# Kernel optimization log

Hardware: AMD Instinct MI355X
Metric: run time of the kernel (lower is better)

Reference implementation:

```python
import jax, jax.numpy as jnp
import numpy as np

N_NODES = 100000
N_EDGES = 1600000  # undirected edges (incidence rows)
F_IN, HID, N_CLS = 500, 256, 40
K_ITERS = 5
LAMBDA1 = 3.0
LAMBDA2 = 3.0


def setup_inputs() -> dict:
    key = jax.random.key(0)
    k1, k2, k3, k4, k5 = jax.random.split(key, 5)
    x = jax.random.normal(k1, (N_NODES, F_IN), dtype=jnp.float32)
    W1 = jax.random.normal(k2, (F_IN, HID), dtype=jnp.float32) * 0.05
    W2 = jax.random.normal(k3, (HID, N_CLS), dtype=jnp.float32) * 0.05
    src = jax.random.randint(k4, (N_EDGES,), 0, N_NODES, dtype=jnp.int32)
    off = jax.random.randint(k5, (N_EDGES,), 1, N_NODES, dtype=jnp.int32)
    dst = (src + off) % N_NODES  # avoid self-edges
    return {"x": x, "W1": W1, "W2": W2, "src": src, "dst": dst}


def reference(x, W1, W2, src, dst):
    N = x.shape[0]
    # --- MLP (eval mode: dropout is identity) ---
    h = jnp.maximum(x @ W1, 0.0)
    h = h @ W2  # [N, C]

    # --- gcn_norm: A_hat = D^{-1/2}(A + I)D^{-1/2}, deg from A + I ---
    rows = jnp.concatenate([src, dst])  # symmetric adjacency
    cols = jnp.concatenate([dst, src])
    deg = jax.ops.segment_sum(jnp.ones(rows.shape[0], x.dtype), rows,
                              num_segments=N) + 1.0
    dis = deg ** -0.5  # deg_inv_sqrt, [N]
    edge_val = dis[rows] * dis[cols]
    self_val = dis * dis

    def spmm(v):  # A_hat @ v
        return (jax.ops.segment_sum(edge_val[:, None] * v[cols], rows,
                                    num_segments=N) + self_val[:, None] * v)

    # normalized incidence: inc[e, src]=dis[src], inc[e, dst]=-dis[dst]
    def inc_t(z):  # inc.T @ z -> [N, C]
        return dis[:, None] * (jax.ops.segment_sum(z, src, num_segments=N)
                               - jax.ops.segment_sum(z, dst, num_segments=N))

    def inc(v):  # inc @ v -> [E, C]
        vs = dis[:, None] * v
        return vs[src] - vs[dst]

    gamma = 1.0 / (1.0 + LAMBDA2)
    beta = 1.0 / (2.0 * gamma)

    hh = h
    xc = h
    z = jnp.zeros((src.shape[0], h.shape[1]), h.dtype)
    for _ in range(K_ITERS):
        y = gamma * hh + (1.0 - gamma) * spmm(xc)
        x_bar = y - gamma * inc_t(z)
        z_bar = z + beta * inc(x_bar)
        # L21 proximal projection: clamp row norms at lambda1
        rn = jnp.linalg.norm(z_bar, axis=1)
        scale = jnp.where(rn > 0,
                          jnp.minimum(rn, LAMBDA1) / jnp.where(rn > 0, rn, 1.0),
                          0.0)
        z = scale[:, None] * z_bar
        xc = y - gamma * inc_t(z)
        # F.dropout with training=False is identity
    return jax.nn.log_softmax(xc, axis=1)
```

## Files before the change

kernel.cpp:

```cpp
#include <hip/hip_runtime.h>
#include <hip/hip_fp16.h>
#include <math.h>

#define NN 100000
#define NE 1600000
#define FIN 500
#define FINP 512
#define HID 256
#define NC 40
#define NC2 20
#define KIT 5
#define L1P 3.0f
#define GAM 0.25f
#define BET 2.0f
#define OMG 0.75f
#define PADH2 32

typedef short bf16x8 __attribute__((ext_vector_type(8)));
typedef unsigned short us8 __attribute__((ext_vector_type(8)));
typedef float f32x4 __attribute__((ext_vector_type(4)));

__device__ inline void split_bf16(float x, unsigned short& hi, unsigned short& lo) {
    unsigned u = __float_as_uint(x);
    hi = (unsigned short)(u >> 16);
    float r = x - __uint_as_float(u & 0xFFFF0000u);
    unsigned ur = __float_as_uint(r);
    ur += 0x8000u + ((ur >> 16) & 1u);
    lo = (unsigned short)(ur >> 16);
}

__global__ void k_hist(const int* __restrict__ s, const int* __restrict__ d, int* cs, int* cd) {
    int e = blockIdx.x * 256 + threadIdx.x;
    if (e < NE) { atomicAdd(&cs[s[e]], 1); atomicAdd(&cd[d[e]], 1); }
}

__global__ void k_scan1(const int* __restrict__ cnt, int* rp, int* bs) {
    __shared__ int sm[1024];
    int i = blockIdx.x * 1024 + threadIdx.x;
    int v = (i < NN) ? cnt[i] : 0;
    sm[threadIdx.x] = v;
    __syncthreads();
    for (int off = 1; off < 1024; off <<= 1) {
        int t = (threadIdx.x >= off) ? sm[threadIdx.x - off] : 0;
        __syncthreads();
        sm[threadIdx.x] += t;
        __syncthreads();
    }
    if (i < NN) rp[i] = sm[threadIdx.x] - v;
    if (threadIdx.x == 1023) bs[blockIdx.x] = sm[1023];
}

__global__ void k_scan2(int* bs, int nb) {
    if (threadIdx.x == 0 && blockIdx.x == 0) {
        int run = 0;
        for (int j = 0; j < nb; j++) { int t = bs[j]; bs[j] = run; run += t; }
    }
}

__global__ void k_scan3(int* rp, const int* __restrict__ bs, int total) {
    int i = blockIdx.x * 1024 + threadIdx.x;
    if (i < NN) rp[i] += bs[blockIdx.x];
    if (i == 0) rp[NN] = total;
}

__global__ void k_dis(const int* __restrict__ cs, const int* __restrict__ cd, float* __restrict__ dis) {
    int n = blockIdx.x * 256 + threadIdx.x;
    if (n < NN) dis[n] = rsqrtf((float)(cs[n] + cd[n]) + 1.0f);
}

__global__ void k_fillp(const int* __restrict__ s, const int* __restrict__ d,
                        const int* __restrict__ rps, const int* __restrict__ rpd,
                        int* curs, int* curd,
                        int* sa, int* sb, int* pd, int* da) {
    int e = blockIdx.x * 256 + threadIdx.x;
    if (e < NE) {
        int a = s[e], b = d[e];
        int i = rps[a] + atomicAdd(&curs[a], 1);
        int j = rpd[b] + atomicAdd(&curd[b], 1);
        sa[i] = a; sb[i] = b; pd[i] = j; da[j] = a;
    }
}

__global__ void k_splitW(const float* __restrict__ W1, unsigned short* __restrict__ Wh,
                         unsigned short* __restrict__ Wl) {
    int idx = blockIdx.x * 256 + threadIdx.x;
    if (idx >= HID * FINP) return;
    int kk = idx >> 8;
    int n  = idx & (HID - 1);
    float v = (kk < FIN) ? W1[(size_t)kk * HID + n] : 0.f;
    unsigned short h, l;
    split_bf16(v, h, l);
    Wh[(size_t)n * FINP + kk] = h;
    Wl[(size_t)n * FINP + kk] = l;
}

__global__ __launch_bounds__(256) void k_gemm1m(const float* __restrict__ X,
                                                const unsigned short* __restrict__ W1h,
                                                const unsigned short* __restrict__ W1l,
                                                float* __restrict__ H1) {
    __shared__ unsigned short Ah[32][40], Al[32][40];
    __shared__ unsigned short Bh[256][40], Bl[256][40];
    const int t = threadIdx.x;
    const int rblk = blockIdx.x * 32;
    const int lane = t & 63, wv = t >> 6;
    const int mw = (wv >> 1) * 16;
    const int nw = (wv & 1) * 128;
    const int l15 = lane & 15, kg = lane >> 4;

    f32x4 acc[8];
    #pragma unroll
    for (int i = 0; i < 8; i++) acc[i] = (f32x4){0.f, 0.f, 0.f, 0.f};

    const int ar = t >> 3;
    const int ak = (t & 7) * 4;
    const int grow = rblk + ar;

    for (int ks = 0; ks < 16; ks++) {
        const int k0 = ks * 32;
        __syncthreads();
        {
            float4 v = make_float4(0.f, 0.f, 0.f, 0.f);
            if (grow < NN && k0 + ak < FIN)
                v = *(const float4*)(X + (size_t)grow * FIN + k0 + ak);
            ushort4 h4, l4;
            split_bf16(v.x, h4.x, l4.x); split_bf16(v.y, h4.y, l4.y);
            split_bf16(v.z, h4.z, l4.z); split_bf16(v.w, h4.w, l4.w);
            *(ushort4*)&Ah[ar][ak] = h4;
            *(ushort4*)&Al[ar][ak] = l4;
        }
        {
            const size_t wb = (size_t)t * FINP + k0;
            #pragma unroll
            for (int q = 0; q < 4; q++) {
                *(us8*)&Bh[t][q * 8] = *(const us8*)&W1h[wb + q * 8];
                *(us8*)&Bl[t][q * 8] = *(const us8*)&W1l[wb + q * 8];
            }
        }
        __syncthreads();
        bf16x8 a_h = *(const bf16x8*)&Ah[mw + l15][kg * 8];
        bf16x8 a_l = *(const bf16x8*)&Al[mw + l15][kg * 8];
        #pragma unroll
        for (int nt = 0; nt < 8; nt++) {
            int n = nw + nt * 16 + l15;
            bf16x8 b_h = *(const bf16x8*)&Bh[n][kg * 8];
            bf16x8 b_l = *(const bf16x8*)&Bl[n][kg * 8];
            acc[nt] = __builtin_amdgcn_mfma_f32_16x16x32_bf16(a_h, b_h, acc[nt], 0, 0, 0);
            acc[nt] = __builtin_amdgcn_mfma_f32_16x16x32_bf16(a_h, b_l, acc[nt], 0, 0, 0);
            acc[nt] = __builtin_amdgcn_mfma_f32_16x16x32_bf16(a_l, b_h, acc[nt], 0, 0, 0);
        }
    }
    const int orow = rblk + mw + kg * 4;
    #pragma unroll
    for (int reg = 0; reg < 4; reg++) {
        int gr = orow + reg;
        if (gr < NN) {
            #pragma unroll
            for (int nt = 0; nt < 8; nt++)
                H1[(size_t)gr * HID + nw + nt * 16 + l15] = fmaxf(acc[nt][reg], 0.f);
        }
    }
}

__global__ __launch_bounds__(256) void k_gemm2(const float* __restrict__ H1,
                                               const float* __restrict__ W2,
                                               const float* __restrict__ dis,
                                               float* __restrict__ hh, __half2* __restrict__ xg2) {
    __shared__ float w2s[HID * NC];
    for (int i = threadIdx.x; i < HID * NC; i += 256) w2s[i] = W2[i];
    __syncthreads();
    int wave = threadIdx.x >> 6, lane = threadIdx.x & 63;
    int n = blockIdx.x * 4 + wave;
    if (n >= NN) return;
    if (lane < NC) {
        const float* hr = H1 + (size_t)n * HID;
        float acc = 0.f;
        #pragma unroll 4
        for (int k = 0; k < HID; k += 4) {
            float4 h4 = *(const float4*)(hr + k);
            acc = fmaf(h4.x, w2s[(k + 0) * NC + lane], acc);
            acc = fmaf(h4.y, w2s[(k + 1) * NC + lane], acc);
            acc = fmaf(h4.z, w2s[(k + 2) * NC + lane], acc);
            acc = fmaf(h4.w, w2s[(k + 3) * NC + lane], acc);
        }
        hh[(size_t)n * NC + lane] = acc;
        ((__half*)xg2)[(size_t)n * (2 * PADH2) + lane] = __float2half_rn(dis[n] * acc);
    }
}

__global__ __launch_bounds__(256) void k_ynew(const int* __restrict__ rps, const int* __restrict__ rpd,
                                              const int* __restrict__ sb, const int* __restrict__ da,
                                              const float* __restrict__ dis, const float2* __restrict__ hh2,
                                              const float2* __restrict__ S2, const __half2* __restrict__ xg2,
                                              float2* __restrict__ y2, __half2* __restrict__ xbs2) {
    int wave = threadIdx.x >> 6, lane = threadIdx.x & 63;
    int g = lane >> 5, sl = lane & 31;
    int n = blockIdx.x * 4 + wave;
    if (n >= NN) return;
    bool act = sl < NC2;
    float accx = 0.f, accy = 0.f;

    int p = rps[n] + g, e0 = rps[n + 1];
    for (; p + 2 < e0; p += 4) {
        int c0 = sb[p], c1 = sb[p + 2];
        if (act) {
            float2 v0 = __half22float2(xg2[(size_t)c0 * PADH2 + sl]);
            float2 v1 = __half22float2(xg2[(size_t)c1 * PADH2 + sl]);
            accx += v0.x + v1.x; accy += v0.y + v1.y;
        }
    }
    if (p < e0) {
        int c = sb[p];
        if (act) {
            float2 v = __half22float2(xg2[(size_t)c * PADH2 + sl]);
            accx += v.x; accy += v.y;
        }
    }
    p = rpd[n] + g; e0 = rpd[n + 1];
    for (; p + 2 < e0; p += 4) {
        int c0 = da[p], c1 = da[p + 2];
        if (act) {
            float2 v0 = __half22float2(xg2[(size_t)c0 * PADH2 + sl]);
            float2 v1 = __half22float2(xg2[(size_t)c1 * PADH2 + sl]);
            accx += v0.x + v1.x; accy += v0.y + v1.y;
        }
    }
    if (p < e0) {
        int c = da[p];
        if (act) {
            float2 v = __half22float2(xg2[(size_t)c * PADH2 + sl]);
            accx += v.x; accy += v.y;
        }
    }
    accx += __shfl_xor(accx, 32);
    accy += __shfl_xor(accy, 32);
    if (act && g == 0) {
        float2 self = __half22float2(xg2[(size_t)n * PADH2 + sl]);
        accx += self.x; accy += self.y;
        size_t b2 = (size_t)n * NC2 + sl;
        float dn = dis[n];
        float2 h = hh2[b2], Sv = S2[b2];
        float yx = GAM * h.x + OMG * dn * accx;
        float yy = GAM * h.y + OMG * dn * accy;
        y2[b2] = make_float2(yx, yy);
        xbs2[(size_t)n * PADH2 + sl] = __float22half2_rn(
            make_float2(dn * (yx - GAM * dn * Sv.x), dn * (yy - GAM * dn * Sv.y)));
    }
}

__global__ __launch_bounds__(256) void k_zup(const int* __restrict__ sa, const int* __restrict__ sb,
                                             const int* __restrict__ pd, const __half2* __restrict__ xbs2,
                                             __half2* __restrict__ zs2, __half2* __restrict__ zd2, int use_z) {
    int wid = (blockIdx.x * 256 + threadIdx.x) >> 6;
    int lane = threadIdx.x & 63;
    int g = lane >> 5, sl = lane & 31;
    long i = (long)wid * 2 + g;
    if (i >= NE) return;
    int a = sa[i], b = sb[i], j = pd[i];
    float zx = 0.f, zy = 0.f;
    bool act = sl < NC2;
    if (act) {
        float2 ia = __half22float2(xbs2[(size_t)a * PADH2 + sl]);
        float2 ib = __half22float2(xbs2[(size_t)b * PADH2 + sl]);
        float2 zv = make_float2(0.f, 0.f);
        if (use_z) zv = __half22float2(zs2[(size_t)i * NC2 + sl]);
        zx = zv.x + BET * (ia.x - ib.x);
        zy = zv.y + BET * (ia.y - ib.y);
    }
    float n2 = zx * zx + zy * zy;
    #pragma unroll
    for (int off = 1; off < 32; off <<= 1) n2 += __shfl_xor(n2, off, 32);
    float rn = sqrtf(n2);
    float sc = (rn > L1P) ? (L1P / rn) : 1.0f;
    if (act) {
        __half2 hv = __float22half2_rn(make_float2(zx * sc, zy * sc));
        zs2[(size_t)i * NC2 + sl] = hv;
        zd2[(size_t)j * NC2 + sl] = hv;
    }
}

__global__ __launch_bounds__(256) void k_scx(const int* __restrict__ rps, const int* __restrict__ rpd,
                                             const __half2* __restrict__ zs2, const __half2* __restrict__ zd2,
                                             const float2* __restrict__ y2, const float* __restrict__ dis,
                                             float2* __restrict__ S2, float2* __restrict__ xc2,
                                             __half2* __restrict__ xg2) {
    int wave = threadIdx.x >> 6, lane = threadIdx.x & 63;
    int g = lane >> 5, sl = lane & 31;
    int n = blockIdx.x * 4 + wave;
    if (n >= NN) return;
    bool act = sl < NC2;
    float accx = 0.f, accy = 0.f;

    int p = rps[n] + g, e0 = rps[n + 1];
    for (; p + 2 < e0; p += 4) {
        if (act) {
            float2 v0 = __half22float2(zs2[(size_t)p * NC2 + sl]);
            float2 v1 = __half22float2(zs2[(size_t)(p + 2) * NC2 + sl]);
            accx += v0.x + v1.x; accy += v0.y + v1.y;
        }
    }
    if (p < e0 && act) {
        float2 v = __half22float2(zs2[(size_t)p * NC2 + sl]);
        accx += v.x; accy += v.y;
    }
    p = rpd[n] + g; e0 = rpd[n + 1];
    for (; p + 2 < e0; p += 4) {
        if (act) {
            float2 v0 = __half22float2(zd2[(size_t)p * NC2 + sl]);
            float2 v1 = __half22float2(zd2[(size_t)(p + 2) * NC2 + sl]);
            accx -= v0.x + v1.x; accy -= v0.y + v1.y;
        }
    }
    if (p < e0 && act) {
        float2 v = __half22float2(zd2[(size_t)p * NC2 + sl]);
        accx -= v.x; accy -= v.y;
    }
    accx += __shfl_xor(accx, 32);
    accy += __shfl_xor(accy, 32);
    if (act && g == 0) {
        size_t b2 = (size_t)n * NC2 + sl;
        float dn = dis[n];
        float2 yv = y2[b2];
        float vx = yv.x - GAM * dn * accx;
        float vy = yv.y - GAM * dn * accy;
        S2[b2] = make_float2(accx, accy);
        xc2[b2] = make_float2(vx, vy);
        xg2[(size_t)n * PADH2 + sl] = __float22half2_rn(make_float2(dn * vx, dn * vy));
    }
}

__global__ __launch_bounds__(256) void k_lsm(const float* __restrict__ xc, float* __restrict__ out) {
    int wave = threadIdx.x >> 6, lane = threadIdx.x & 63;
    int n = blockIdx.x * 4 + wave;
    if (n >= NN) return;
    float v = (lane < NC) ? xc[(size_t)n * NC + lane] : -INFINITY;
    float m = v;
    #pragma unroll
    for (int off = 1; off < 64; off <<= 1) m = fmaxf(m, __shfl_xor(m, off));
    float ex = (lane < NC) ? expf(v - m) : 0.f;
    float ssum = ex;
    #pragma unroll
    for (int off = 1; off < 64; off <<= 1) ssum += __shfl_xor(ssum, off);
    if (lane < NC) out[(size_t)n * NC + lane] = v - m - logf(ssum);
}

extern "C" void kernel_launch(void* const* d_in, const int* in_sizes, int n_in,
                              void* d_out, int out_size, void* d_ws, size_t ws_size,
                              hipStream_t stream) {
    const float* x  = (const float*)d_in[0];
    const float* W1 = (const float*)d_in[1];
    const float* W2 = (const float*)d_in[2];
    const int* src  = (const int*)d_in[3];
    const int* dst  = (const int*)d_in[4];
    float* out = (float*)d_out;

    char* w = (char*)d_ws;
    auto alloc = [&](size_t bytes) { char* p = w; w += (bytes + 255) & ~(size_t)255; return p; };
    float* dis   = (float*)alloc((size_t)NN * 4);
    int*   cs    = (int*)  alloc((size_t)NN * 4);
    int*   cd    = (int*)  alloc((size_t)NN * 4);
    int*   curs  = (int*)  alloc((size_t)NN * 4);
    int*   curd  = (int*)  alloc((size_t)NN * 4);
    int*   rps   = (int*)  alloc((size_t)(NN + 1) * 4);
    int*   rpd   = (int*)  alloc((size_t)(NN + 1) * 4);
    int*   bs    = (int*)  alloc(1024 * 4);
    int*   sa    = (int*)  alloc((size_t)NE * 4);
    int*   sb    = (int*)  alloc((size_t)NE * 4);
    int*   pd    = (int*)  alloc((size_t)NE * 4);
    int*   da    = (int*)  alloc((size_t)NE * 4);
    unsigned short* W1h = (unsigned short*)alloc((size_t)HID * FINP * 2);
    unsigned short* W1l = (unsigned short*)alloc((size_t)HID * FINP * 2);
    float* hh    = (float*)alloc((size_t)NN * NC * 4);
    float* xc    = (float*)alloc((size_t)NN * NC * 4);
    float* yb    = (float*)alloc((size_t)NN * NC * 4);
    float* S     = (float*)alloc((size_t)NN * NC * 4);
    __half2* xg  = (__half2*)alloc((size_t)NN * PADH2 * 4);
    __half2* xbs = (__half2*)alloc((size_t)NN * PADH2 * 4);
    __half2* zs  = (__half2*)alloc((size_t)NE * NC2 * 4);
    __half2* zd  = (__half2*)alloc((size_t)NE * NC2 * 4);
    float* h1    = (float*)zs;

    hipMemsetAsync(cs, 0, (size_t)NN * 4, stream);
    hipMemsetAsync(cd, 0, (size_t)NN * 4, stream);
    hipMemsetAsync(curs, 0, (size_t)NN * 4, stream);
    hipMemsetAsync(curd, 0, (size_t)NN * 4, stream);
    k_hist<<<(NE + 255) / 256, 256, 0, stream>>>(src, dst, cs, cd);
    int nb = (NN + 1023) / 1024;
    k_scan1<<<nb, 1024, 0, stream>>>(cs, rps, bs);
    k_scan2<<<1, 64, 0, stream>>>(bs, nb);
    k_scan3<<<nb, 1024, 0, stream>>>(rps, bs, NE);
    k_scan1<<<nb, 1024, 0, stream>>>(cd, rpd, bs);
    k_scan2<<<1, 64, 0, stream>>>(bs, nb);
    k_scan3<<<nb, 1024, 0, stream>>>(rpd, bs, NE);
    k_dis<<<(NN + 255) / 256, 256, 0, stream>>>(cs, cd, dis);
    k_fillp<<<(NE + 255) / 256, 256, 0, stream>>>(src, dst, rps, rpd, curs, curd, sa, sb, pd, da);

    k_splitW<<<(HID * FINP + 255) / 256, 256, 0, stream>>>(W1, W1h, W1l);
    k_gemm1m<<<(NN + 31) / 32, 256, 0, stream>>>(x, W1h, W1l, h1);
    k_gemm2<<<(NN + 3) / 4, 256, 0, stream>>>(h1, W2, dis, hh, xg);

    hipMemsetAsync(S, 0, (size_t)NN * NC * 4, stream);
    int zblocks = (int)(((size_t)NE / 2 + 3) / 4);
    for (int t = 0; t < KIT; t++) {
        k_ynew<<<(NN + 3) / 4, 256, 0, stream>>>(rps, rpd, sb, da, dis, (const float2*)hh,
                                                 (const float2*)S, xg, (float2*)yb, xbs);
        k_zup<<<zblocks, 256, 0, stream>>>(sa, sb, pd, xbs, zs, zd, t > 0 ? 1 : 0);
        k_scx<<<(NN + 3) / 4, 256, 0, stream>>>(rps, rpd, zs, zd, (const float2*)yb, dis,
                                                (float2*)S, (float2*)xc, xg);
    }
    k_lsm<<<(NN + 3) / 4, 256, 0, stream>>>(xc, out);
}
```

Baseline: 3.612 ms.

## Use fragment-major LDS layout in GEMM1 and unroll gather loops deeper

Reorganises the shared-memory tiles of the split-bf16 MFMA GEMM into a fragment-major layout, so each lane's 8-element MFMA operand is read contiguously across lanes, aiming to reduce LDS bank conflicts compared with the padded row-major layout. It also unrolls the neighbour-gather loops in the ynew and scx sparse kernels to four loads per iteration, to raise memory-level parallelism on the irregular gathers. The A-tile writes now go through ushort4 halves, which may bring their own bank patterns, and the extra unrolling raises register use.

```diff
diff --git a/kernel.cpp b/kernel.cpp
--- a/kernel.cpp
+++ b/kernel.cpp
@@ -98,13 +98,13 @@
                                                 const unsigned short* __restrict__ W1h,
                                                 const unsigned short* __restrict__ W1l,
                                                 float* __restrict__ H1) {
-    __shared__ unsigned short Ah[32][40], Al[32][40];
-    __shared__ unsigned short Bh[256][40], Bl[256][40];
+    __shared__ us8 AFh[2][4][16], AFl[2][4][16];
+    __shared__ us8 BFh[2][8][4][16], BFl[2][8][4][16];
     const int t = threadIdx.x;
     const int rblk = blockIdx.x * 32;
     const int lane = t & 63, wv = t >> 6;
-    const int mw = (wv >> 1) * 16;
-    const int nw = (wv & 1) * 128;
+    const int mh = wv >> 1;
+    const int nh = wv & 1;
     const int l15 = lane & 15, kg = lane >> 4;
 
     f32x4 acc[8];
@@ -112,44 +112,46 @@
     for (int i = 0; i < 8; i++) acc[i] = (f32x4){0.f, 0.f, 0.f, 0.f};
 
     const int ar = t >> 3;
-    const int ak = (t & 7) * 4;
+    const int koct = t & 7;
+    const int akg = koct >> 1, ahalf = koct & 1;
     const int grow = rblk + ar;
+    const int bnh = t >> 7, bnt = (t & 127) >> 4, bl15 = t & 15;
 
     for (int ks = 0; ks < 16; ks++) {
         const int k0 = ks * 32;
         __syncthreads();
         {
             float4 v = make_float4(0.f, 0.f, 0.f, 0.f);
-            if (grow < NN && k0 + ak < FIN)
-                v = *(const float4*)(X + (size_t)grow * FIN + k0 + ak);
+            if (grow < NN && k0 + koct * 4 < FIN)
+                v = *(const float4*)(X + (size_t)grow * FIN + k0 + koct * 4);
             ushort4 h4, l4;
             split_bf16(v.x, h4.x, l4.x); split_bf16(v.y, h4.y, l4.y);
             split_bf16(v.z, h4.z, l4.z); split_bf16(v.w, h4.w, l4.w);
-            *(ushort4*)&Ah[ar][ak] = h4;
-            *(ushort4*)&Al[ar][ak] = l4;
+            ((ushort4*)&AFh[ar >> 4][akg][ar & 15])[ahalf] = h4;
+            ((ushort4*)&AFl[ar >> 4][akg][ar & 15])[ahalf] = l4;
         }
         {
             const size_t wb = (size_t)t * FINP + k0;
             #pragma unroll
             for (int q = 0; q < 4; q++) {
-                *(us8*)&Bh[t][q * 8] = *(const us8*)&W1h[wb + q * 8];
-                *(us8*)&Bl[t][q * 8] = *(const us8*)&W1l[wb + q * 8];
+                BFh[bnh][bnt][q][bl15] = *(const us8*)&W1h[wb + q * 8];
+                BFl[bnh][bnt][q][bl15] = *(const us8*)&W1l[wb + q * 8];
             }
         }
         __syncthreads();
-        bf16x8 a_h = *(const bf16x8*)&Ah[mw + l15][kg * 8];
-        bf16x8 a_l = *(const bf16x8*)&Al[mw + l15][kg * 8];
+        bf16x8 a_h = *(const bf16x8*)&AFh[mh][kg][l15];
+        bf16x8 a_l = *(const bf16x8*)&AFl[mh][kg][l15];
         #pragma unroll
         for (int nt = 0; nt < 8; nt++) {
-            int n = nw + nt * 16 + l15;
-            bf16x8 b_h = *(const bf16x8*)&Bh[n][kg * 8];
-            bf16x8 b_l = *(const bf16x8*)&Bl[n][kg * 8];
+            bf16x8 b_h = *(const bf16x8*)&BFh[nh][nt][kg][l15];
+            bf16x8 b_l = *(const bf16x8*)&BFl[nh][nt][kg][l15];
             acc[nt] = __builtin_amdgcn_mfma_f32_16x16x32_bf16(a_h, b_h, acc[nt], 0, 0, 0);
             acc[nt] = __builtin_amdgcn_mfma_f32_16x16x32_bf16(a_h, b_l, acc[nt], 0, 0, 0);
             acc[nt] = __builtin_amdgcn_mfma_f32_16x16x32_bf16(a_l, b_h, acc[nt], 0, 0, 0);
         }
     }
-    const int orow = rblk + mw + kg * 4;
+    const int orow = rblk + mh * 16 + kg * 4;
+    const int nw = nh * 128;
     #pragma unroll
     for (int reg = 0; reg < 4; reg++) {
         int gr = orow + reg;
@@ -199,36 +201,36 @@
     bool act = sl < NC2;
     float accx = 0.f, accy = 0.f;
 
-    int p = rps[n] + g, e0 = rps[n + 1];
-    for (; p + 2 < e0; p += 4) {
-        int c0 = sb[p], c1 = sb[p + 2];
-        if (act) {
-            float2 v0 = __half22float2(xg2[(size_t)c0 * PADH2 + sl]);
-            float2 v1 = __half22float2(xg2[(size_t)c1 * PADH2 + sl]);
-            accx += v0.x + v1.x; accy += v0.y + v1.y;
-        }
-    }
-    if (p < e0) {
-        int c = sb[p];
-        if (act) {
-            float2 v = __half22float2(xg2[(size_t)c * PADH2 + sl]);
-            accx += v.x; accy += v.y;
-        }
-    }
-    p = rpd[n] + g; e0 = rpd[n + 1];
-    for (; p + 2 < e0; p += 4) {
-        int c0 = da[p], c1 = da[p + 2];
-        if (act) {
-            float2 v0 = __half22float2(xg2[(size_t)c0 * PADH2 + sl]);
-            float2 v1 = __half22float2(xg2[(size_t)c1 * PADH2 + sl]);
-            accx += v0.x + v1.x; accy += v0.y + v1.y;
-        }
-    }
-    if (p < e0) {
-        int c = da[p];
-        if (act) {
-            float2 v = __half22float2(xg2[(size_t)c * PADH2 + sl]);
-            accx += v.x; accy += v.y;
+    #pragma unroll
+    for (int side = 0; side < 2; side++) {
+        const int* __restrict__ idx = side ? da : sb;
+        int p = (side ? rpd[n] : rps[n]) + g;
+        int e0 = side ? rpd[n + 1] : rps[n + 1];
+        for (; p + 6 < e0; p += 8) {
+            int c0 = idx[p], c1 = idx[p + 2], c2 = idx[p + 4], c3 = idx[p + 6];
+            if (act) {
+                float2 v0 = __half22float2(xg2[(size_t)c0 * PADH2 + sl]);
+                float2 v1 = __half22float2(xg2[(size_t)c1 * PADH2 + sl]);
+                float2 v2 = __half22float2(xg2[(size_t)c2 * PADH2 + sl]);
+                float2 v3 = __half22float2(xg2[(size_t)c3 * PADH2 + sl]);
+                accx += (v0.x + v1.x) + (v2.x + v3.x);
+                accy += (v0.y + v1.y) + (v2.y + v3.y);
+            }
+        }
+        for (; p + 2 < e0; p += 4) {
+            int c0 = idx[p], c1 = idx[p + 2];
+            if (act) {
+                float2 v0 = __half22float2(xg2[(size_t)c0 * PADH2 + sl]);
+                float2 v1 = __half22float2(xg2[(size_t)c1 * PADH2 + sl]);
+                accx += v0.x + v1.x; accy += v0.y + v1.y;
+            }
+        }
+        if (p < e0) {
+            int c = idx[p];
+            if (act) {
+                float2 v = __half22float2(xg2[(size_t)c * PADH2 + sl]);
+                accx += v.x; accy += v.y;
+            }
         }
     }
     accx += __shfl_xor(accx, 32);
@@ -291,9 +293,19 @@
     float accx = 0.f, accy = 0.f;
 
     int p = rps[n] + g, e0 = rps[n + 1];
+    for (; p + 6 < e0; p += 8) {
+        if (act) {
+            float2 v0 = __half22float2(zs2[(size_t)(p + 0) * NC2 + sl]);
+            float2 v1 = __half22float2(zs2[(size_t)(p + 2) * NC2 + sl]);
+            float2 v2 = __half22float2(zs2[(size_t)(p + 4) * NC2 + sl]);
+            float2 v3 = __half22float2(zs2[(size_t)(p + 6) * NC2 + sl]);
+            accx += (v0.x + v1.x) + (v2.x + v3.x);
+            accy += (v0.y + v1.y) + (v2.y + v3.y);
+        }
+    }
     for (; p + 2 < e0; p += 4) {
         if (act) {
-            float2 v0 = __half22float2(zs2[(size_t)p * NC2 + sl]);
+            float2 v0 = __half22float2(zs2[(size_t)(p + 0) * NC2 + sl]);
             float2 v1 = __half22float2(zs2[(size_t)(p + 2) * NC2 + sl]);
             accx += v0.x + v1.x; accy += v0.y + v1.y;
         }
@@ -303,9 +315,19 @@
         accx += v.x; accy += v.y;
     }
     p = rpd[n] + g; e0 = rpd[n + 1];
+    for (; p + 6 < e0; p += 8) {
+        if (act) {
+            float2 v0 = __half22float2(zd2[(size_t)(p + 0) * NC2 + sl]);
+            float2 v1 = __half22float2(zd2[(size_t)(p + 2) * NC2 + sl]);
+            float2 v2 = __half22float2(zd2[(size_t)(p + 4) * NC2 + sl]);
+            float2 v3 = __half22float2(zd2[(size_t)(p + 6) * NC2 + sl]);
+            accx -= (v0.x + v1.x) + (v2.x + v3.x);
+            accy -= (v0.y + v1.y) + (v2.y + v3.y);
+        }
+    }
     for (; p + 2 < e0; p += 4) {
         if (act) {
-            float2 v0 = __half22float2(zd2[(size_t)p * NC2 + sl]);
+            float2 v0 = __half22float2(zd2[(size_t)(p + 0) * NC2 + sl]);
             float2 v1 = __half22float2(zd2[(size_t)(p + 2) * NC2 + sl]);
             accx -= v0.x + v1.x; accy -= v0.y + v1.y;
         }
```

Measured after the change: 3.362 ms. 6.9% less time.
